# Optimization experiments

Hardware: AMD Instinct MI355X
Metric: run time of the kernel (lower is better)

Reference implementation:

```python
import jax, jax.numpy as jnp
import numpy as np

B, H, E, D = 16384, 1024, 64, 128  # batch, hidden, nb_entities, wh_units==we_units


def setup_inputs() -> dict:
    key = jax.random.key(0)
    k0, k1, k2 = jax.random.split(key, 3)
    hidden_state = jax.random.normal(k0, (B, H), dtype=jnp.float32)
    # Wh: Dense(wh_units) acting on H -> D
    Wh_w = jax.random.normal(k1, (H, D), dtype=jnp.float32) * 0.02
    Wh_b = jnp.zeros((D,), dtype=jnp.float32)
    # We: nb_entities separate Dense(we_units), stacked into one [E, D, D] tensor
    We_w = jax.random.normal(k2, (E, D, D), dtype=jnp.float32) * 0.02
    We_b = jnp.zeros((E, D), dtype=jnp.float32)
    return {"hidden_state": hidden_state, "Wh_w": Wh_w, "Wh_b": Wh_b,
            "We_w": We_w, "We_b": We_b}


def reference(hidden_state, Wh_w, Wh_b, We_w, We_b):
    # reduced_dimentionality = Wh(hidden_state)            [B, D]
    r = hidden_state @ Wh_w + Wh_b
    # per-entity Dense loop + concat + transpose == one batched GEMM -> [B, E, D]
    logits = jnp.einsum('bk,ekd->bed', r, We_w) + We_b[None, :, :]
    outputs = jax.nn.softmax(logits, axis=-1)               # [B, E, D]
    # second pass: We[i] applied to outputs[:, i, :]       [B, E, D]
    vt = jnp.einsum('bek,ekd->bed', outputs, We_w) + We_b[None, :, :]
    # transpose to [B, D, E] then reduce_sum over E == sum over entity axis
    result = vt.sum(axis=1)                                 # [B, D]
    return (outputs, result)
```

## Files before the change

### kernel.cpp

```cpp
#include <hip/hip_runtime.h>
#include <hip/hip_bf16.h>

typedef __attribute__((ext_vector_type(8))) short short8;
typedef __attribute__((ext_vector_type(4))) float f32x4;
typedef __attribute__((ext_vector_type(4))) unsigned int uint4v;
typedef __attribute__((ext_vector_type(2))) unsigned int uint2v;

#define NB 16384
#define NH 1024
#define NE 64
#define ND 128
#define BR 32

static __device__ __forceinline__ unsigned short f2b(float x) {
  unsigned int u = __builtin_bit_cast(unsigned int, x);
  unsigned int r = (u + 0x7fffu + ((u >> 16) & 1u)) >> 16;
  return (unsigned short)r;
}
static __device__ __forceinline__ float b2f_lo(unsigned int u) {
  return __builtin_bit_cast(float, u << 16);
}
static __device__ __forceinline__ float b2f_hi(unsigned int u) {
  return __builtin_bit_cast(float, u & 0xffff0000u);
}

static __device__ __forceinline__ void bar_sync() {
  __builtin_amdgcn_sched_barrier(0);
  asm volatile("s_waitcnt lgkmcnt(0)" ::: "memory");
  __builtin_amdgcn_sched_barrier(0);
  __builtin_amdgcn_s_barrier();
  __builtin_amdgcn_sched_barrier(0);
}

static __device__ __forceinline__ int swz(int row, int col) {
  return (row << 7) + ((((col >> 3) ^ (row & 15)) << 3) | (col & 7));
}

__global__ __launch_bounds__(256, 1) void k0_prep(
    const float* __restrict__ Wh_w, const float* __restrict__ We_w,
    const float* __restrict__ We_b,
    unsigned short* __restrict__ WeT, unsigned short* __restrict__ WhT,
    float* __restrict__ bsum)
{
  __shared__ float tile[32][33];
  const int bid = blockIdx.x, t = threadIdx.x;
  const int i = t >> 5, j = t & 31;
  if (bid < 1024) {
    const int e = bid >> 4, tr = (bid >> 2) & 3, tc = bid & 3;
    const float* src = We_w + (size_t)e * 16384;
#pragma unroll
    for (int k = 0; k < 4; ++k)
      tile[i + 8 * k][j] = src[(size_t)(tr * 32 + i + 8 * k) * 128 + tc * 32 + j];
    __syncthreads();
    unsigned short* dst = WeT + (size_t)e * 16384;
#pragma unroll
    for (int k = 0; k < 4; ++k) {
      int row = i + 8 * k;
      dst[(size_t)(tc * 32 + row) * 128 + tr * 32 + j] = f2b(tile[j][row]);
    }
  } else if (bid < 1152) {
    const int tb = bid - 1024, tr = tb >> 2, tc = tb & 3;
#pragma unroll
    for (int k = 0; k < 4; ++k)
      tile[i + 8 * k][j] = Wh_w[(size_t)(tr * 32 + i + 8 * k) * 128 + tc * 32 + j];
    __syncthreads();
#pragma unroll
    for (int k = 0; k < 4; ++k) {
      int row = i + 8 * k;
      WhT[(size_t)(tc * 32 + row) * 1024 + tr * 32 + j] = f2b(tile[j][row]);
    }
  } else {
    if (t < 128) {
      float s = 0.f;
      for (int e = 0; e < 64; ++e) s += We_b[e * 128 + t];
      bsum[t] = s;
    }
  }
}

struct SmemK2 {
  union {
    unsigned short Pst[2][BR * 128];
    float obuf[BR * 128];
  };
  unsigned short r_lds[BR * 128];
  float sms[2][4][BR];
  float invr[2][BR];
};

static __device__ __forceinline__ void load_we_frags(
    short8 (&f)[2][4], f32x4 (&bias)[2],
    const unsigned short* __restrict__ WeT, const float* __restrict__ We_b,
    int e, int w, int c, int g)
{
  const unsigned short* base = WeT + (size_t)e * (ND * ND);
#pragma unroll
  for (int mf = 0; mf < 2; ++mf) {
    const unsigned short* rowp = base + (size_t)(16 * (2 * w + mf) + c) * ND + 8 * g;
#pragma unroll
    for (int ks = 0; ks < 4; ++ks)
      f[mf][ks] = *(const short8*)(rowp + 32 * ks);
    bias[mf] = *(const f32x4*)(We_b + e * ND + 32 * w + 16 * mf + 4 * g);
  }
}

static __device__ __forceinline__ void store_p_slice(
    const SmemK2& sm, float* __restrict__ outP,
    int brow0, int e_prev, int sp, int t)
{
#pragma unroll
  for (int it = 0; it < 4; ++it) {
    const int flat = it * 1024 + t * 4;
    const int row = flat >> 7;
    const int col = flat & 127;
    const float inv = sm.invr[sp][row];
    uint2v u = *(const uint2v*)(&sm.Pst[sp][swz(row, col)]);
    f32x4 v;
    v[0] = b2f_lo(u[0]) * inv; v[1] = b2f_hi(u[0]) * inv;
    v[2] = b2f_lo(u[1]) * inv; v[3] = b2f_hi(u[1]) * inv;
    float* dst = outP + ((size_t)(brow0 + row) * NE + e_prev) * ND + col;
    __builtin_nontemporal_store(v, (f32x4*)dst);
  }
}

static __device__ __forceinline__ void entity_body(
    int i, int en, int ep, int brow0, int w, int c, int g, int t,
    short8 (&cur)[2][4], short8 (&nxt)[2][4],
    f32x4 (&bcur)[2], f32x4 (&bnxt)[2], f32x4 (&acc2)[2][2],
    const unsigned short* __restrict__ WeT, const float* __restrict__ We_b,
    float* __restrict__ outP, SmemK2& sm)
{
  const int si = i & 1, sp = si ^ 1;
  load_we_frags(nxt, bnxt, WeT, We_b, en, w, c, g);
  __builtin_amdgcn_sched_barrier(0);
  if (i > 0) store_p_slice(sm, outP, brow0, ep, sp, t);
  __builtin_amdgcn_sched_barrier(0);
  f32x4 acc1[2][2];
#pragma unroll
  for (int mf = 0; mf < 2; ++mf)
#pragma unroll
    for (int nf = 0; nf < 2; ++nf) acc1[mf][nf] = (f32x4){0.f, 0.f, 0.f, 0.f};
#pragma unroll
  for (int ks = 0; ks < 4; ++ks) {
    short8 b1[2];
#pragma unroll
    for (int nf = 0; nf < 2; ++nf)
      b1[nf] = *(const short8*)(&sm.r_lds[swz(16 * nf + c, 8 * g + 32 * ks)]);
#pragma unroll
    for (int mf = 0; mf < 2; ++mf)
#pragma unroll
      for (int nf = 0; nf < 2; ++nf)
        acc1[mf][nf] = __builtin_amdgcn_mfma_f32_16x16x32_bf16(
            cur[mf][ks], b1[nf], acc1[mf][nf], 0, 0, 0);
  }
#pragma unroll
  for (int mf = 0; mf < 2; ++mf)
#pragma unroll
    for (int nf = 0; nf < 2; ++nf) acc1[mf][nf] += bcur[mf];
  float s[2] = {0.f, 0.f};
#pragma unroll
  for (int nf = 0; nf < 2; ++nf) {
#pragma unroll
    for (int mf = 0; mf < 2; ++mf)
#pragma unroll
      for (int r = 0; r < 4; ++r) {
        float p = __expf(acc1[mf][nf][r]);
        acc1[mf][nf][r] = p;
        s[nf] += p;
      }
    s[nf] += __shfl_xor(s[nf], 16);
    s[nf] += __shfl_xor(s[nf], 32);
  }
  if (g == 0) {
    sm.sms[si][w][c] = s[0];
    sm.sms[si][w][16 + c] = s[1];
  }
#pragma unroll
  for (int mf = 0; mf < 2; ++mf)
#pragma unroll
    for (int nf = 0; nf < 2; ++nf) {
      f32x4 p = acc1[mf][nf];
      unsigned int lo = (unsigned)f2b(p[0]) | ((unsigned)f2b(p[1]) << 16);
      unsigned int hi = (unsigned)f2b(p[2]) | ((unsigned)f2b(p[3]) << 16);
      uint2v pk = {lo, hi};
      *(uint2v*)(&sm.Pst[si][swz(16 * nf + c, 32 * w + 16 * mf + 4 * g)]) = pk;
    }
  bar_sync();
  f32x4 inv4[2];
#pragma unroll
  for (int mf2 = 0; mf2 < 2; ++mf2) {
    const int b0 = 16 * mf2 + 4 * g;
    f32x4 sv = *(const f32x4*)(&sm.sms[si][0][b0]);
    sv += *(const f32x4*)(&sm.sms[si][1][b0]);
    sv += *(const f32x4*)(&sm.sms[si][2][b0]);
    sv += *(const f32x4*)(&sm.sms[si][3][b0]);
#pragma unroll
    for (int r = 0; r < 4; ++r) inv4[mf2][r] = __builtin_amdgcn_rcpf(sv[r]);
  }
  if (g == 0) {
#pragma unroll
    for (int nf = 0; nf < 2; ++nf) {
      const int b = 16 * nf + c;
      float st = sm.sms[si][0][b] + sm.sms[si][1][b] +
                 sm.sms[si][2][b] + sm.sms[si][3][b];
      sm.invr[si][b] = __builtin_amdgcn_rcpf(st);
    }
  }
  f32x4 eacc[2][2];
#pragma unroll
  for (int mf2 = 0; mf2 < 2; ++mf2)
#pragma unroll
    for (int n = 0; n < 2; ++n) eacc[mf2][n] = (f32x4){0.f, 0.f, 0.f, 0.f};
#pragma unroll
  for (int ks2 = 0; ks2 < 4; ++ks2) {
    short8 a2[2];
#pragma unroll
    for (int mf2 = 0; mf2 < 2; ++mf2)
      a2[mf2] = *(const short8*)(&sm.Pst[si][swz(16 * mf2 + c, 8 * g + 32 * ks2)]);
#pragma unroll
    for (int mf2 = 0; mf2 < 2; ++mf2)
#pragma unroll
      for (int n = 0; n < 2; ++n)
        eacc[mf2][n] = __builtin_amdgcn_mfma_f32_16x16x32_bf16(
            a2[mf2], cur[n][ks2], eacc[mf2][n], 0, 0, 0);
  }
#pragma unroll
  for (int mf2 = 0; mf2 < 2; ++mf2)
#pragma unroll
    for (int n = 0; n < 2; ++n)
      acc2[mf2][n] += eacc[mf2][n] * inv4[mf2];
}

__global__ __launch_bounds__(256, 2) void k2_main(
    const float* __restrict__ hidden, const unsigned short* __restrict__ WhT,
    const float* __restrict__ Wh_b, const unsigned short* __restrict__ WeT,
    const float* __restrict__ We_b, const float* __restrict__ bsum,
    float* __restrict__ outP, float* __restrict__ outR)
{
  __shared__ SmemK2 sm;
  const int t = threadIdx.x;
  const int w = t >> 6, l = t & 63, c = l & 15, g = l >> 4;
  const int lb = (blockIdx.x & 7) * 64 + (blockIdx.x >> 3);
  const int brow0 = lb * BR;
  const int e0 = (((lb >> 6) + lb) & 7) << 3;

  short8 wa[2][4], wb[2][4];
  f32x4 ba[2], bb[2];
  load_we_frags(wa, ba, WeT, We_b, e0, w, c, g);

  {
    f32x4 pacc[2][2];
#pragma unroll
    for (int mf = 0; mf < 2; ++mf)
#pragma unroll
      for (int nf = 0; nf < 2; ++nf) pacc[mf][nf] = (f32x4){0.f, 0.f, 0.f, 0.f};
    const float* h0p = hidden + (size_t)(brow0 + c) * NH;
    const float* h1p = hidden + (size_t)(brow0 + 16 + c) * NH;
    const unsigned short* wa0 = WhT + (size_t)(32 * w + c) * NH;
    const unsigned short* wa1 = WhT + (size_t)(32 * w + 16 + c) * NH;
#pragma unroll 2
    for (int ks = 0; ks < 32; ++ks) {
      const int k0 = 8 * g + 32 * ks;
      f32x4 ha = *(const f32x4*)(h0p + k0);
      f32x4 hb = *(const f32x4*)(h0p + k0 + 4);
      f32x4 hc = *(const f32x4*)(h1p + k0);
      f32x4 hd = *(const f32x4*)(h1p + k0 + 4);
      short8 bf0, bf1;
      bf0[0] = (short)f2b(ha[0]); bf0[1] = (short)f2b(ha[1]);
      bf0[2] = (short)f2b(ha[2]); bf0[3] = (short)f2b(ha[3]);
      bf0[4] = (short)f2b(hb[0]); bf0[5] = (short)f2b(hb[1]);
      bf0[6] = (short)f2b(hb[2]); bf0[7] = (short)f2b(hb[3]);
      bf1[0] = (short)f2b(hc[0]); bf1[1] = (short)f2b(hc[1]);
      bf1[2] = (short)f2b(hc[2]); bf1[3] = (short)f2b(hc[3]);
      bf1[4] = (short)f2b(hd[0]); bf1[5] = (short)f2b(hd[1]);
      bf1[6] = (short)f2b(hd[2]); bf1[7] = (short)f2b(hd[3]);
      short8 af0 = *(const short8*)(wa0 + k0);
      short8 af1 = *(const short8*)(wa1 + k0);
      pacc[0][0] = __builtin_amdgcn_mfma_f32_16x16x32_bf16(af0, bf0, pacc[0][0], 0, 0, 0);
      pacc[0][1] = __builtin_amdgcn_mfma_f32_16x16x32_bf16(af0, bf1, pacc[0][1], 0, 0, 0);
      pacc[1][0] = __builtin_amdgcn_mfma_f32_16x16x32_bf16(af1, bf0, pacc[1][0], 0, 0, 0);
      pacc[1][1] = __builtin_amdgcn_mfma_f32_16x16x32_bf16(af1, bf1, pacc[1][1], 0, 0, 0);
    }
#pragma unroll
    for (int mf = 0; mf < 2; ++mf) {
      const int d0 = 32 * w + 16 * mf + 4 * g;
      f32x4 bias = *(const f32x4*)(Wh_b + d0);
#pragma unroll
      for (int nf = 0; nf < 2; ++nf) {
        f32x4 v = pacc[mf][nf] + bias;
        unsigned int lo = (unsigned)f2b(v[0]) | ((unsigned)f2b(v[1]) << 16);
        unsigned int hi = (unsigned)f2b(v[2]) | ((unsigned)f2b(v[3]) << 16);
        uint2v pk = {lo, hi};
        *(uint2v*)(&sm.r_lds[swz(16 * nf + c, d0)]) = pk;
      }
    }
  }
  const float bs0 = bsum[32 * w + c];
  const float bs1 = bsum[32 * w + 16 + c];
  bar_sync();

  f32x4 acc2[2][2];
#pragma unroll
  for (int i = 0; i < 2; ++i)
#pragma unroll
    for (int j = 0; j < 2; ++j) acc2[i][j] = (f32x4){0.f, 0.f, 0.f, 0.f};

#pragma unroll 1
  for (int i = 0; i < NE; i += 2) {
    const int eB = (e0 + i + 1) & 63, eC = (e0 + i + 2) & 63;
    const int pA = (e0 + i + 63) & 63, pB = (e0 + i) & 63;
    entity_body(i,     eB, pA, brow0, w, c, g, t,
                wa, wb, ba, bb, acc2, WeT, We_b, outP, sm);
    entity_body(i + 1, eC, pB, brow0, w, c, g, t,
                wb, wa, bb, ba, acc2, WeT, We_b, outP, sm);
  }
  store_p_slice(sm, outP, brow0, (e0 + 63) & 63, 1, t);

  bar_sync();
#pragma unroll
  for (int mf2 = 0; mf2 < 2; ++mf2)
#pragma unroll
    for (int n = 0; n < 2; ++n) {
      float bs = n ? bs1 : bs0;
#pragma unroll
      for (int r = 0; r < 4; ++r)
        sm.obuf[(16 * mf2 + 4 * g + r) * ND + 32 * w + 16 * n + c] =
            acc2[mf2][n][r] + bs;
    }
  bar_sync();
  {
    const int orow = t >> 5, ocol = (t & 31) * 4;
#pragma unroll
    for (int it = 0; it < 4; ++it) {
      const int row = orow + 8 * it;
      f32x4 v = *(const f32x4*)(&sm.obuf[row * ND + ocol]);
      __builtin_nontemporal_store(
          v, (f32x4*)(outR + (size_t)(brow0 + row) * ND + ocol));
    }
  }
}

extern "C" void kernel_launch(void* const* d_in, const int* in_sizes, int n_in,
                              void* d_out, int out_size, void* d_ws, size_t ws_size,
                              hipStream_t stream)
{
  (void)in_sizes; (void)n_in; (void)out_size; (void)ws_size;
  const float* hidden = (const float*)d_in[0];
  const float* Wh_w   = (const float*)d_in[1];
  const float* Wh_b   = (const float*)d_in[2];
  const float* We_w   = (const float*)d_in[3];
  const float* We_b   = (const float*)d_in[4];
  float* outP = (float*)d_out;
  float* outR = outP + (size_t)NB * NE * ND;

  char* ws = (char*)d_ws;
  unsigned short* WeT = (unsigned short*)(ws);
  unsigned short* WhT = (unsigned short*)(ws + 2097152);
  float* bsum         = (float*)(ws + 2097152 + 262144);

  k0_prep<<<1153, 256, 0, stream>>>(Wh_w, We_w, We_b, WeT, WhT, bsum);
  k2_main<<<512, 256, 0, stream>>>(hidden, WhT, Wh_b, WeT, We_b, bsum, outP, outR);
}
```

Baseline: 247.4 us.

## Split hidden-projection GEMM into a separate kernel staging r in workspace

Moves the hidden_state @ Wh projection out of the main fused kernel into a new k1_rgemm kernel that writes r as bf16 to a global workspace buffer. The main kernel now only loads its 32x128 r tile from global memory into LDS before the entity loop, which reduces its register pressure and front-end latency. In exchange it adds a kernel launch and a 4 MB round trip through global memory, and the new kernel uses a different warp-to-tile mapping.

```diff
diff --git a/kernel.cpp b/kernel.cpp
--- a/kernel.cpp
+++ b/kernel.cpp
@@ -75,6 +75,46 @@
       for (int e = 0; e < 64; ++e) s += We_b[e * 128 + t];
       bsum[t] = s;
     }
+  }
+}
+
+__global__ __launch_bounds__(256, 2) void k1_rgemm(
+    const float* __restrict__ hidden, const unsigned short* __restrict__ WhT,
+    const float* __restrict__ Wh_b, unsigned short* __restrict__ r_g)
+{
+  const int t = threadIdx.x;
+  const int w = t >> 6, l = t & 63, c = l & 15, g = l >> 4;
+  const int bg = w & 1, dh = w >> 1;
+  const int b = blockIdx.x * 32 + 16 * bg + c;
+  const float* hrow = hidden + (size_t)b * NH;
+  f32x4 acc[4];
+#pragma unroll
+  for (int mf = 0; mf < 4; ++mf) acc[mf] = (f32x4){0.f, 0.f, 0.f, 0.f};
+#pragma unroll 2
+  for (int ks = 0; ks < 32; ++ks) {
+    const int k0 = 8 * g + 32 * ks;
+    f32x4 h0 = *(const f32x4*)(hrow + k0);
+    f32x4 h1 = *(const f32x4*)(hrow + k0 + 4);
+    short8 bf;
+    bf[0] = (short)f2b(h0[0]); bf[1] = (short)f2b(h0[1]);
+    bf[2] = (short)f2b(h0[2]); bf[3] = (short)f2b(h0[3]);
+    bf[4] = (short)f2b(h1[0]); bf[5] = (short)f2b(h1[1]);
+    bf[6] = (short)f2b(h1[2]); bf[7] = (short)f2b(h1[3]);
+#pragma unroll
+    for (int mf = 0; mf < 4; ++mf) {
+      short8 af = *(const short8*)(WhT + (size_t)(64 * dh + 16 * mf + c) * NH + k0);
+      acc[mf] = __builtin_amdgcn_mfma_f32_16x16x32_bf16(af, bf, acc[mf], 0, 0, 0);
+    }
+  }
+#pragma unroll
+  for (int mf = 0; mf < 4; ++mf) {
+    const int d0 = 64 * dh + 16 * mf + 4 * g;
+    f32x4 bias = *(const f32x4*)(Wh_b + d0);
+    f32x4 v = acc[mf] + bias;
+    unsigned int lo = (unsigned)f2b(v[0]) | ((unsigned)f2b(v[1]) << 16);
+    unsigned int hi = (unsigned)f2b(v[2]) | ((unsigned)f2b(v[3]) << 16);
+    uint2v pk = {lo, hi};
+    *(uint2v*)(r_g + (size_t)b * ND + d0) = pk;
   }
 }
 
@@ -232,8 +272,7 @@
 }
 
 __global__ __launch_bounds__(256, 2) void k2_main(
-    const float* __restrict__ hidden, const unsigned short* __restrict__ WhT,
-    const float* __restrict__ Wh_b, const unsigned short* __restrict__ WeT,
+    const unsigned short* __restrict__ r_g, const unsigned short* __restrict__ WeT,
     const float* __restrict__ We_b, const float* __restrict__ bsum,
     float* __restrict__ outP, float* __restrict__ outR)
 {
@@ -244,66 +283,24 @@
   const int brow0 = lb * BR;
   const int e0 = (((lb >> 6) + lb) & 7) << 3;
 
+  for (int i = t; i < BR * 16; i += 256) {
+    int row = i >> 4, ch = i & 15;
+    uint4v v = *(const uint4v*)(r_g + (size_t)(brow0 + row) * ND + ch * 8);
+    *(uint4v*)(&sm.r_lds[swz(row, ch * 8)]) = v;
+  }
+  const float bs0 = bsum[32 * w + c];
+  const float bs1 = bsum[32 * w + 16 + c];
+
+  f32x4 acc2[2][2];
+#pragma unroll
+  for (int i = 0; i < 2; ++i)
+#pragma unroll
+    for (int j = 0; j < 2; ++j) acc2[i][j] = (f32x4){0.f, 0.f, 0.f, 0.f};
+
   short8 wa[2][4], wb[2][4];
   f32x4 ba[2], bb[2];
   load_we_frags(wa, ba, WeT, We_b, e0, w, c, g);
-
-  {
-    f32x4 pacc[2][2];
-#pragma unroll
-    for (int mf = 0; mf < 2; ++mf)
-#pragma unroll
-      for (int nf = 0; nf < 2; ++nf) pacc[mf][nf] = (f32x4){0.f, 0.f, 0.f, 0.f};
-    const float* h0p = hidden + (size_t)(brow0 + c) * NH;
-    const float* h1p = hidden + (size_t)(brow0 + 16 + c) * NH;
-    const unsigned short* wa0 = WhT + (size_t)(32 * w + c) * NH;
-    const unsigned short* wa1 = WhT + (size_t)(32 * w + 16 + c) * NH;
-#pragma unroll 2
-    for (int ks = 0; ks < 32; ++ks) {
-      const int k0 = 8 * g + 32 * ks;
-      f32x4 ha = *(const f32x4*)(h0p + k0);
-      f32x4 hb = *(const f32x4*)(h0p + k0 + 4);
-      f32x4 hc = *(const f32x4*)(h1p + k0);
-      f32x4 hd = *(const f32x4*)(h1p + k0 + 4);
-      short8 bf0, bf1;
-      bf0[0] = (short)f2b(ha[0]); bf0[1] = (short)f2b(ha[1]);
-      bf0[2] = (short)f2b(ha[2]); bf0[3] = (short)f2b(ha[3]);
-      bf0[4] = (short)f2b(hb[0]); bf0[5] = (short)f2b(hb[1]);
-      bf0[6] = (short)f2b(hb[2]); bf0[7] = (short)f2b(hb[3]);
-      bf1[0] = (short)f2b(hc[0]); bf1[1] = (short)f2b(hc[1]);
-      bf1[2] = (short)f2b(hc[2]); bf1[3] = (short)f2b(hc[3]);
-      bf1[4] = (short)f2b(hd[0]); bf1[5] = (short)f2b(hd[1]);
-      bf1[6] = (short)f2b(hd[2]); bf1[7] = (short)f2b(hd[3]);
-      short8 af0 = *(const short8*)(wa0 + k0);
-      short8 af1 = *(const short8*)(wa1 + k0);
-      pacc[0][0] = __builtin_amdgcn_mfma_f32_16x16x32_bf16(af0, bf0, pacc[0][0], 0, 0, 0);
-      pacc[0][1] = __builtin_amdgcn_mfma_f32_16x16x32_bf16(af0, bf1, pacc[0][1], 0, 0, 0);
-      pacc[1][0] = __builtin_amdgcn_mfma_f32_16x16x32_bf16(af1, bf0, pacc[1][0], 0, 0, 0);
-      pacc[1][1] = __builtin_amdgcn_mfma_f32_16x16x32_bf16(af1, bf1, pacc[1][1], 0, 0, 0);
-    }
-#pragma unroll
-    for (int mf = 0; mf < 2; ++mf) {
-      const int d0 = 32 * w + 16 * mf + 4 * g;
-      f32x4 bias = *(const f32x4*)(Wh_b + d0);
-#pragma unroll
-      for (int nf = 0; nf < 2; ++nf) {
-        f32x4 v = pacc[mf][nf] + bias;
-        unsigned int lo = (unsigned)f2b(v[0]) | ((unsigned)f2b(v[1]) << 16);
-        unsigned int hi = (unsigned)f2b(v[2]) | ((unsigned)f2b(v[3]) << 16);
-        uint2v pk = {lo, hi};
-        *(uint2v*)(&sm.r_lds[swz(16 * nf + c, d0)]) = pk;
-      }
-    }
-  }
-  const float bs0 = bsum[32 * w + c];
-  const float bs1 = bsum[32 * w + 16 + c];
   bar_sync();
-
-  f32x4 acc2[2][2];
-#pragma unroll
-  for (int i = 0; i < 2; ++i)
-#pragma unroll
-    for (int j = 0; j < 2; ++j) acc2[i][j] = (f32x4){0.f, 0.f, 0.f, 0.f};
 
 #pragma unroll 1
   for (int i = 0; i < NE; i += 2) {
@@ -356,8 +353,10 @@
   char* ws = (char*)d_ws;
   unsigned short* WeT = (unsigned short*)(ws);
   unsigned short* WhT = (unsigned short*)(ws + 2097152);
-  float* bsum         = (float*)(ws + 2097152 + 262144);
+  unsigned short* r_g = (unsigned short*)(ws + 2097152 + 262144);
+  float* bsum         = (float*)(ws + 2097152 + 262144 + 4194304);
 
   k0_prep<<<1153, 256, 0, stream>>>(Wh_w, We_w, We_b, WeT, WhT, bsum);
-  k2_main<<<512, 256, 0, stream>>>(hidden, WhT, Wh_b, WeT, We_b, bsum, outP, outR);
-}
+  k1_rgemm<<<512, 256, 0, stream>>>(hidden, WhT, Wh_b, r_g);
+  k2_main<<<512, 256, 0, stream>>>(r_g, WeT, We_b, bsum, outP, outR);
+}
```

Measured after the change: 250.1 us. About the same (+1.1%).
